# Kernel tuning notes

Hardware: AMD Instinct MI355X
Metric: run time of the kernel (lower is better)

The kernel has to match this reference:

```python
import jax, jax.numpy as jnp
import numpy as np
from jax import lax

THETA = 1.0      # neuron['theta']
TAU_SR = 10.0    # neuron['tauSr'] (SRM synaptic time constant)
TAU_RHO = 1.0    # surrogate-gradient width
SCALE_RHO = 1.0  # surrogate-gradient scale
T_SIM = 100      # simulation['tSample']


def srm_kernel(T, dtype=jnp.float32):
    t = jnp.arange(T, dtype=dtype)
    return (t / TAU_SR) * jnp.exp(1.0 - t / TAU_SR)  # eps(0)=0, peak 1 at t=tau


def psp(x, eps):
    """Causal temporal filter along last axis: y[t] = sum_k eps[k] * x[t-k]."""
    shape = x.shape
    T = shape[-1]
    xf = x.reshape(-1, 1, T)
    k = eps[::-1].reshape(1, 1, T)
    y = lax.conv_general_dilated(xf, k, (1,), [(T - 1, 0)],
                                 dimension_numbers=('NCH', 'OIH', 'NCH'))
    return y.reshape(shape)


def spike(u):
    return (u >= THETA).astype(u.dtype)


def conv_t(x, w, pad):
    """Per-timestep 2D conv. x:[B,C,H,W,T], w:[O,I,kh,kw] -> [B,O,H',W',T]."""
    B, C, H, W, T = x.shape
    xt = jnp.moveaxis(x, -1, 1).reshape(B * T, C, H, W)
    y = lax.conv_general_dilated(xt, w, (1, 1), [(pad, pad), (pad, pad)],
                                 dimension_numbers=('NCHW', 'OIHW', 'NCHW'))
    O, Ho, Wo = y.shape[1], y.shape[2], y.shape[3]
    return jnp.moveaxis(y.reshape(B, T, O, Ho, Wo), 1, -1)


def pool2(x):
    """SLAYER pool: 2x2 sum with fixed weight 1.1. x:[B,C,H,W,T]."""
    B, C, H, W, T = x.shape
    xr = x.reshape(B, C, H // 2, 2, W // 2, 2, T)
    return 1.1 * xr.sum(axis=(3, 5))


def dense_t(x, w):
    """x:[B,C,H,W,T] flattened over CHW; w:[O, C*H*W] -> [B,O,T]."""
    B = x.shape[0]
    T = x.shape[-1]
    xf = x.reshape(B, -1, T)
    return jnp.einsum('bit,oi->bot', xf, w)


def setup_inputs() -> dict:
    key = jax.random.key(0)
    k = jax.random.split(key, 6)
    img = jax.random.uniform(k[0], (32, 1, 28, 28), dtype=jnp.float32)
    rand_u = jax.random.uniform(k[1], (32, 1, 28, 28, T_SIM), dtype=jnp.float32)
    w1 = jax.random.normal(k[2], (16, 1, 5, 5), dtype=jnp.float32) * 0.2
    w2 = jax.random.normal(k[3], (32, 16, 5, 5), dtype=jnp.float32) * 0.05
    wf1 = jax.random.normal(k[4], (410, 1568), dtype=jnp.float32) * 0.05
    wf2 = jax.random.normal(k[5], (10, 410), dtype=jnp.float32) * 0.05
    return {"img": img, "rand_u": rand_u, "w1": w1, "w2": w2, "wf1": wf1, "wf2": wf2}


def reference(img, rand_u, w1, w2, wf1, wf2):
    eps = srm_kernel(T_SIM, img.dtype)
    # rate encoding: Bernoulli spikes with p = pixel intensity
    x = (rand_u < img[..., None]).astype(img.dtype)          # [B,1,28,28,T]
    x = spike(psp(conv_t(x, w1, 2), eps))                    # [B,16,28,28,T]
    x = spike(psp(pool2(x), eps))                            # [B,16,14,14,T]
    x = spike(psp(conv_t(x, w2, 2), eps))                    # [B,32,14,14,T]
    x = spike(psp(pool2(x), eps))                            # [B,32,7,7,T]
    x = spike(psp(dense_t(x, wf1), eps))                     # [B,410,T]
    x = spike(psp(jnp.einsum('bit,oi->bot', x, wf2), eps))   # [B,10,T]
    return x
```

## Files before the change

kernel.cpp:

```cpp
#include <hip/hip_runtime.h>


namespace {
constexpr int B = 32, T = 100;
constexpr double A1 = 0.90483741803595957;
constexpr double CE = 0.27182818284590452;
constexpr double SC39 = 549755813888.0;
constexpr double INV39 = 1.0 / 549755813888.0;

constexpr size_t OFF_M1 = 0;
constexpr size_t OFF_M2 = OFF_M1 + (size_t)B * T * 28 * 4;
constexpr size_t OFF_S4 = OFF_M2 + (size_t)B * T * 224 * 4;
constexpr size_t OFF_D5 = OFF_S4 + (size_t)B * T * 1568;
constexpr size_t OFF_S5 = OFF_D5 + (size_t)B * T * 410 * 8;
constexpr size_t OFF_D6 = OFF_S5 + (size_t)B * T * 410;
constexpr size_t OFF_BP = OFF_D6 + (size_t)B * T * 10 * 8;
constexpr size_t OFF_AP = OFF_D5;
}

using i32x4 = __attribute__((ext_vector_type(4))) int;
using i32x16 = __attribute__((ext_vector_type(16))) int;

__global__ void k_encode_pack(const float* __restrict__ img, const float* __restrict__ ru,
                              unsigned int* __restrict__ m1) {
  int i = blockIdx.x * 256 + threadIdx.x;
  if (i >= B * 28 * T) return;
  int t = i % T;
  int y = (i / T) % 28;
  int b = i / (T * 28);
  unsigned int m = 0;
  const float* rb = ru + ((size_t)b * 784 + y * 28) * T + t;
  const float* ib = img + b * 784 + y * 28;
  for (int x = 0; x < 28; x++) {
    m |= (rb[(size_t)x * T] < ib[x]) ? (1u << x) : 0u;
  }
  m1[((size_t)b * T + t) * 28 + y] = m;
}

__global__ __launch_bounds__(256) void k_conv1(const unsigned int* __restrict__ m1,
                                               const float* __restrict__ w1,
                                               unsigned int* __restrict__ m2) {
  __shared__ double lut[160];
  __shared__ unsigned int mrow[2][32];
  __shared__ unsigned char spk[784];
  __shared__ unsigned char spkP[2][196];
  int o = blockIdx.x % 16, b = blockIdx.x / 16;
  int tid = threadIdx.x;
  if (tid < 160) {
    int dy = tid / 32, f = tid % 32;
    double v = 0.0;
    const float* wb = w1 + o * 25 + dy * 5;
#pragma unroll
    for (int dx = 0; dx < 5; dx++)
      if ((f >> dx) & 1) v += (double)wb[dx];
    lut[tid] = v;
  }
  if (tid < 32) {
    mrow[0][tid] = 0;
    mrow[1][tid] = 0;
  }
  int y = tid / 7, xg = tid % 7;
  int py = tid / 14, px = tid % 14;
  bool act = tid < 196;
  double g1[4] = {0, 0, 0, 0}, g2[4] = {0, 0, 0, 0};
  double p1 = 0.0, p2 = 0.0;
  const unsigned int* m1b = m1 + (size_t)b * T * 28;
  if (tid < 28) mrow[0][tid + 2] = m1b[tid] << 2;
  __syncthreads();
  for (int t = 0; t < T; t++) {
    int cur = t & 1, nxt = cur ^ 1;
    bool dold = (tid < 28) && (t + 1 < T);
    unsigned int ldv = 0;
    if (dold) ldv = m1b[(t + 1) * 28 + tid] << 2;
    if (act) {
      double s0 = 0, s1 = 0, s2 = 0, s3 = 0;
      int xb = xg * 4;
      const unsigned int* mc = mrow[cur];
#pragma unroll
      for (int dy = 0; dy < 5; dy++) {
        unsigned int m = mc[y + dy];
        const double* ld = lut + dy * 32;
        s0 += ld[(m >> (xb + 0)) & 31];
        s1 += ld[(m >> (xb + 1)) & 31];
        s2 += ld[(m >> (xb + 2)) & 31];
        s3 += ld[(m >> (xb + 3)) & 31];
      }
      g1[0] = s0 + A1 * g1[0]; g2[0] = g1[0] + A1 * g2[0];
      g1[1] = s1 + A1 * g1[1]; g2[1] = g1[1] + A1 * g2[1];
      g1[2] = s2 + A1 * g1[2]; g2[2] = g1[2] + A1 * g2[2];
      g1[3] = s3 + A1 * g1[3]; g2[3] = g1[3] + A1 * g2[3];
      unsigned char* sp = spk + y * 28 + xb;
      sp[0] = (CE * (g2[0] - g1[0]) >= 1.0) ? 1 : 0;
      sp[1] = (CE * (g2[1] - g1[1]) >= 1.0) ? 1 : 0;
      sp[2] = (CE * (g2[2] - g1[2]) >= 1.0) ? 1 : 0;
      sp[3] = (CE * (g2[3] - g1[3]) >= 1.0) ? 1 : 0;
    }
    if (dold) mrow[nxt][tid + 2] = ldv;
    __syncthreads();
    if (act) {
      const unsigned char* r0 = spk + (2 * py) * 28 + 2 * px;
      int sum = (int)r0[0] + (int)r0[1] + (int)r0[28] + (int)r0[29];
      double s = 1.1 * (double)sum;
      p1 = s + A1 * p1;
      p2 = p1 + A1 * p2;
      spkP[cur][tid] = (CE * (p2 - p1) >= 1.0) ? 1 : 0;
    }
    if (tid < 14 && t > 0) {
      unsigned int m = 0;
      const unsigned char* rp = spkP[nxt] + tid * 14;
#pragma unroll
      for (int xx = 0; xx < 14; xx++) m |= ((unsigned int)rp[xx]) << xx;
      m2[((size_t)(b * T + (t - 1)) * 16 + o) * 14 + tid] = m;
    }
    __syncthreads();
  }
  if (tid < 14) {
    unsigned int m = 0;
    const unsigned char* rp = spkP[(T - 1) & 1] + tid * 14;
#pragma unroll
    for (int xx = 0; xx < 14; xx++) m |= ((unsigned int)rp[xx]) << xx;
    m2[((size_t)(b * T + (T - 1)) * 16 + o) * 14 + tid] = m;
  }
}

__global__ void k_limbs(const float* __restrict__ w2, signed char* __restrict__ AP) {
  int i = blockIdx.x * 256 + threadIdx.x;
  if (i >= 32 * 80 * 8) return;
  int dx = i & 7;
  int g = (i >> 3) % 80;
  int o = i / 640;
  int c = g >> 2, r = g & 3, eh = r >> 1, kh = r & 1;
  int lane = kh * 32 + o, e = eh * 8 + dx;
  int ci = g / 5, dy = g % 5;
  float wv = (dx < 5) ? w2[((o * 16 + ci) * 5 + dy) * 5 + dx] : 0.0f;
  long long m = llrint((double)wv * SC39);
#pragma unroll
  for (int j = 0; j < 5; j++) {
    int d = (int)((m + 128) & 255) - 128;
    AP[(size_t)((j * 20 + c) * 64 + lane) * 16 + e] = (signed char)d;
    m = (m - d) >> 8;
  }
}

__global__ __launch_bounds__(256, 1) void k_conv2u(const unsigned int* __restrict__ m2,
                                                   const signed char* __restrict__ AP,
                                                   unsigned char* __restrict__ s4) {
  __shared__ unsigned int maskW[2][2][176];
  __shared__ double part[2][2][2][32][30];
  int yp = blockIdx.x % 7, b = blockIdx.x / 7;
  int y0 = yp * 2;
  int tid = threadIdx.x;
  int w = tid >> 6, l = tid & 63;
  int tp = w >> 1, kg = w & 1;
  int col = l & 31, kh = l >> 5;
  int x = col % 14;
  unsigned int wmask = (col < 28) ? 31u : 0u;
  int half = (col >= 14) ? 1 : 0;
  const unsigned int* m2b = m2 + (size_t)b * T * 224;

  const i32x4* APv = (const i32x4*)AP;
  i32x4 Af[5][10];
#pragma unroll
  for (int j = 0; j < 5; j++)
#pragma unroll
    for (int cl = 0; cl < 10; cl++)
      Af[j][cl] = APv[(size_t)((j * 20) + kg * 10 + cl) * 64 + l];

  int stPos[3] = {-1, -1, -1}, stIdx[3] = {-1, -1, -1};
  if (w < 2) {
#pragma unroll
    for (int pass = 0; pass < 3; pass++) {
      if (pass == 2 && l >= 32) continue;
      int e = pass * 64 + l;
      int H = e / 80, g = e % 80;
      int ci = g / 5, dy = g % 5;
      int iy = y0 - 2 + H + dy;
      stPos[pass] = H * 80 + (g & 1) * 40 + 2 * (g >> 2) + ((g >> 1) & 1);
      if (iy >= 0 && iy < 14) stIdx[pass] = ci * 14 + iy;
    }
  }

  int po = tid / 7, pp = tid % 7;
  bool chainAct = tid < 224;
  double sg1[4] = {0, 0, 0, 0}, sg2[4] = {0, 0, 0, 0};
  double q1 = 0.0, q2 = 0.0;

  if (w < 2) {
#pragma unroll
    for (int pass = 0; pass < 3; pass++) {
      if (stPos[pass] < 0) continue;
      unsigned int v = 0;
      if (stIdx[pass] >= 0) v = m2b[(size_t)w * 224 + stIdx[pass]] << 2;
      maskW[0][w][stPos[pass]] = v;
    }
  }
  __syncthreads();

  for (int grp = 0; grp < 50; grp++) {
    int p = grp & 1, np = p ^ 1;

    unsigned int ld0 = 0, ld1 = 0, ld2 = 0;
    bool doStage = (w < 2) && (grp + 1 < 50);
    if (doStage) {
      size_t tb = (size_t)((grp + 1) * 2 + w) * 224;
      if (stIdx[0] >= 0) ld0 = m2b[tb + stIdx[0]] << 2;
      if (stIdx[1] >= 0) ld1 = m2b[tb + stIdx[1]] << 2;
      if (stIdx[2] >= 0) ld2 = m2b[tb + stIdx[2]] << 2;
    }

    {
      const uint4* mwv = (const uint4*)&maskW[p][tp][0];
      int base4 = half * 20 + kh * 10 + 5 * kg;
      uint4 mk0 = mwv[base4 + 0], mk1 = mwv[base4 + 1], mk2 = mwv[base4 + 2];
      uint4 mk3 = mwv[base4 + 3], mk4 = mwv[base4 + 4];
      i32x16 ac0, ac1, ac2, ac3, ac4;
#pragma unroll
      for (int r = 0; r < 16; r++) { ac0[r] = 0; ac1[r] = 0; ac2[r] = 0; ac3[r] = 0; ac4[r] = 0; }
#pragma unroll
      for (int cl = 0; cl < 10; cl++) {
        uint4 mkv = (cl < 2) ? mk0 : (cl < 4) ? mk1 : (cl < 6) ? mk2 : (cl < 8) ? mk3 : mk4;
        unsigned int ra = (cl & 1) ? mkv.z : mkv.x;
        unsigned int rb = (cl & 1) ? mkv.w : mkv.y;
        unsigned int a5 = (ra >> x) & wmask;
        unsigned int b5 = (rb >> x) & wmask;
        i32x4 bb;
        bb[0] = (int)(((a5 & 15u) * 0x204081u) & 0x01010101u);
        bb[1] = (int)((a5 >> 4) & 1u);
        bb[2] = (int)(((b5 & 15u) * 0x204081u) & 0x01010101u);
        bb[3] = (int)((b5 >> 4) & 1u);
        ac0 = __builtin_amdgcn_mfma_i32_32x32x32_i8(Af[0][cl], bb, ac0, 0, 0, 0);
        ac1 = __builtin_amdgcn_mfma_i32_32x32x32_i8(Af[1][cl], bb, ac1, 0, 0, 0);
        ac2 = __builtin_amdgcn_mfma_i32_32x32x32_i8(Af[2][cl], bb, ac2, 0, 0, 0);
        ac3 = __builtin_amdgcn_mfma_i32_32x32x32_i8(Af[3][cl], bb, ac3, 0, 0, 0);
        ac4 = __builtin_amdgcn_mfma_i32_32x32x32_i8(Af[4][cl], bb, ac4, 0, 0, 0);
      }
      if (col < 28) {
#pragma unroll
        for (int r = 0; r < 16; r++) {
          int R = (r & 3) + 8 * (r >> 2) + 4 * kh;
          int c01 = ac1[r] * 256 + ac0[r];
          int c23 = ac3[r] * 256 + ac2[r];
          double S = ((double)ac4[r] * 65536.0 + (double)c23) * 65536.0 + (double)c01;
          part[p][tp][kg][R][col] = S;
        }
      }
    }

    if (doStage) {
      if (stPos[0] >= 0) maskW[np][w][stPos[0]] = ld0;
      if (stPos[1] >= 0) maskW[np][w][stPos[1]] = ld1;
      if (stPos[2] >= 0) maskW[np][w][stPos[2]] = ld2;
    }
    __syncthreads();

    if (chainAct) {
#pragma unroll
      for (int g = 0; g < 2; g++) {
        const double* a0 = &part[p][g][0][po][2 * pp];
        const double* b0 = &part[p][g][1][po][2 * pp];
        const double* a1 = &part[p][g][0][po][14 + 2 * pp];
        const double* b1 = &part[p][g][1][po][14 + 2 * pp];
        double c0 = (a0[0] + b0[0]) * INV39;
        double c1 = (a0[1] + b0[1]) * INV39;
        double c2 = (a1[0] + b1[0]) * INV39;
        double c3 = (a1[1] + b1[1]) * INV39;
        sg1[0] = c0 + A1 * sg1[0]; sg2[0] = sg1[0] + A1 * sg2[0];
        sg1[1] = c1 + A1 * sg1[1]; sg2[1] = sg1[1] + A1 * sg2[1];
        sg1[2] = c2 + A1 * sg1[2]; sg2[2] = sg1[2] + A1 * sg2[2];
        sg1[3] = c3 + A1 * sg1[3]; sg2[3] = sg1[3] + A1 * sg2[3];
        int sum = ((CE * (sg2[0] - sg1[0]) >= 1.0) ? 1 : 0)
                + ((CE * (sg2[1] - sg1[1]) >= 1.0) ? 1 : 0)
                + ((CE * (sg2[2] - sg1[2]) >= 1.0) ? 1 : 0)
                + ((CE * (sg2[3] - sg1[3]) >= 1.0) ? 1 : 0);
        double s = 1.1 * (double)sum;
        q1 = s + A1 * q1;
        q2 = q1 + A1 * q2;
        s4[(size_t)(b * T + grp * 2 + g) * 1568 + po * 49 + yp * 7 + pp] =
            (CE * (q2 - q1) >= 1.0) ? 1 : 0;
      }
    }
  }
}

__global__ void k_limbs2(const float* __restrict__ wf1, signed char* __restrict__ BP) {
  int i = blockIdx.x * 256 + threadIdx.x;
  if (i >= 13 * 5 * 49 * 64) return;
  int lane = i & 63;
  int fi = i >> 6;
  int c = fi % 49;
  int j = (fi / 49) % 5;
  int ot = fi / 245;
  int o = ot * 32 + (lane & 31);
  int kb = 32 * c + (lane >> 5) * 16;
  int wd[4] = {0, 0, 0, 0};
#pragma unroll
  for (int e = 0; e < 16; e++) {
    float wv = (o < 410) ? wf1[(size_t)o * 1568 + kb + e] : 0.0f;
    long long m = llrint((double)wv * SC39);
    int d = 0;
    for (int jj = 0; jj <= j; jj++) {
      d = (int)((m + 128) & 255) - 128;
      m = (m - d) >> 8;
    }
    wd[e >> 2] |= (d & 255) << ((e & 3) * 8);
  }
  i32x4 v;
  v[0] = wd[0]; v[1] = wd[1]; v[2] = wd[2]; v[3] = wd[3];
  *(i32x4*)(BP + (size_t)i * 16) = v;
}

__global__ __launch_bounds__(256) void k_dense1m(const unsigned char* __restrict__ s4,
                                                 const signed char* __restrict__ BP,
                                                 double* __restrict__ d5) {
  int ot = blockIdx.y;
  int w = threadIdx.x >> 6, l = threadIdx.x & 63;
  int col = l & 31, kh = l >> 5;
  int btTile = blockIdx.x * 4 + w;
  const unsigned char* arow = s4 + (size_t)(btTile * 32 + col) * 1568 + kh * 16;
  const i32x4* bpv = (const i32x4*)BP + (size_t)ot * 245 * 64 + l;
  i32x16 acc0, acc1, acc2, acc3, acc4;
#pragma unroll
  for (int r = 0; r < 16; r++) {
    acc0[r] = 0; acc1[r] = 0; acc2[r] = 0; acc3[r] = 0; acc4[r] = 0;
  }
  for (int c = 0; c < 49; c++) {
    i32x4 a = *(const i32x4*)(arow + 32 * c);
    i32x4 b0 = bpv[(0 * 49 + c) * 64];
    i32x4 b1 = bpv[(1 * 49 + c) * 64];
    i32x4 b2 = bpv[(2 * 49 + c) * 64];
    i32x4 b3 = bpv[(3 * 49 + c) * 64];
    i32x4 b4 = bpv[(4 * 49 + c) * 64];
    acc0 = __builtin_amdgcn_mfma_i32_32x32x32_i8(a, b0, acc0, 0, 0, 0);
    acc1 = __builtin_amdgcn_mfma_i32_32x32x32_i8(a, b1, acc1, 0, 0, 0);
    acc2 = __builtin_amdgcn_mfma_i32_32x32x32_i8(a, b2, acc2, 0, 0, 0);
    acc3 = __builtin_amdgcn_mfma_i32_32x32x32_i8(a, b3, acc3, 0, 0, 0);
    acc4 = __builtin_amdgcn_mfma_i32_32x32x32_i8(a, b4, acc4, 0, 0, 0);
  }
  int o = ot * 32 + col;
  if (o < 410) {
#pragma unroll
    for (int r = 0; r < 16; r++) {
      int R = (r & 3) + 8 * (r >> 2) + 4 * kh;
      double v = ((((double)acc4[r] * 256.0 + (double)acc3[r]) * 256.0 +
                   (double)acc2[r]) * 256.0 + (double)acc1[r]) * 256.0 + (double)acc0[r];
      d5[(size_t)(btTile * 32 + R) * 410 + o] = v * INV39;
    }
  }
}

__global__ void k_psp5(const double* __restrict__ d5, unsigned char* __restrict__ s5) {
  int tid = blockIdx.x * 256 + threadIdx.x;
  if (tid >= B * 410) return;
  int o = tid % 410, b = tid / 410;
  double g1 = 0.0, g2 = 0.0;
  for (int t = 0; t < T; t++) {
    double s = d5[(size_t)(b * T + t) * 410 + o];
    g1 = s + A1 * g1;
    g2 = g1 + A1 * g2;
    s5[(size_t)(b * T + t) * 410 + o] = (CE * (g2 - g1) >= 1.0) ? 1 : 0;
  }
}

__global__ void k_dense2(const unsigned char* __restrict__ s5, const float* __restrict__ wf2,
                         double* __restrict__ d6) {
  int tid = blockIdx.x * 256 + threadIdx.x;
  if (tid >= B * T * 10) return;
  int o = tid % 10, bt = tid / 10;
  const unsigned char* sr = s5 + (size_t)bt * 410;
  const float* wr = wf2 + o * 410;
  double s = 0.0;
  for (int i = 0; i < 410; i++) s += (double)wr[i] * (double)sr[i];
  d6[tid] = s;
}

__global__ void k_psp6(const double* __restrict__ d6, float* __restrict__ out) {
  int tid = blockIdx.x * 256 + threadIdx.x;
  if (tid >= B * 10) return;
  int o = tid % 10, b = tid / 10;
  double g1 = 0.0, g2 = 0.0;
  for (int t = 0; t < T; t++) {
    double s = d6[(size_t)(b * T + t) * 10 + o];
    g1 = s + A1 * g1;
    g2 = g1 + A1 * g2;
    out[(size_t)b * 1000 + o * 100 + t] = (CE * (g2 - g1) >= 1.0) ? 1.0f : 0.0f;
  }
}

extern "C" void kernel_launch(void* const* d_in, const int* in_sizes, int n_in,
                              void* d_out, int out_size, void* d_ws, size_t ws_size,
                              hipStream_t stream) {
  const float* img = (const float*)d_in[0];
  const float* ru = (const float*)d_in[1];
  const float* w1 = (const float*)d_in[2];
  const float* w2 = (const float*)d_in[3];
  const float* wf1 = (const float*)d_in[4];
  const float* wf2 = (const float*)d_in[5];

  unsigned char* ws = (unsigned char*)d_ws;
  unsigned int* m1 = (unsigned int*)(ws + OFF_M1);
  unsigned int* m2 = (unsigned int*)(ws + OFF_M2);
  unsigned char* s4 = ws + OFF_S4;
  double* d5 = (double*)(ws + OFF_D5);
  unsigned char* s5 = ws + OFF_S5;
  double* d6 = (double*)(ws + OFF_D6);
  signed char* AP = (signed char*)(ws + OFF_AP);
  signed char* BP = (signed char*)(ws + OFF_BP);
  float* out = (float*)d_out;

  k_encode_pack<<<(B * 28 * T + 255) / 256, 256, 0, stream>>>(img, ru, m1);
  k_limbs<<<(32 * 80 * 8 + 255) / 256, 256, 0, stream>>>(w2, AP);
  k_limbs2<<<(13 * 5 * 49 * 64 + 255) / 256, 256, 0, stream>>>(wf1, BP);
  k_conv1<<<B * 16, 256, 0, stream>>>(m1, w1, m2);
  k_conv2u<<<B * 7, 256, 0, stream>>>(m2, AP, s4);
  k_dense1m<<<dim3(25, 13), 256, 0, stream>>>(s4, BP, d5);
  k_psp5<<<(B * 410 + 255) / 256, 256, 0, stream>>>(d5, s5);
  k_dense2<<<(B * T * 10 + 255) / 256, 256, 0, stream>>>(s5, wf2, d6);
  k_psp6<<<2, 256, 0, stream>>>(d6, out);
}
```

Before: 404.8 us.

## Split conv2 K-reduction across four wave groups in 512-thread blocks

The conv2 kernel now runs 512 threads per block: eight waves split the channel reduction into four K-quarters per time step instead of two halves. Each wave holds half as many A-fragment registers and issues half as many MFMAs per step. The PSP chain moves to the upper 256 threads and sums four partials. The partial buffer loses its double buffering and an extra barrier is added per iteration, which serializes MFMA work and the chain update, but the aim is more waves in flight and shorter per-wave MFMA sequences.

```diff
diff --git a/kernel.cpp b/kernel.cpp
--- a/kernel.cpp
+++ b/kernel.cpp
@@ -142,16 +142,16 @@
   }
 }
 
-__global__ __launch_bounds__(256, 1) void k_conv2u(const unsigned int* __restrict__ m2,
+__global__ __launch_bounds__(512, 2) void k_conv2w(const unsigned int* __restrict__ m2,
                                                    const signed char* __restrict__ AP,
                                                    unsigned char* __restrict__ s4) {
-  __shared__ unsigned int maskW[2][2][176];
-  __shared__ double part[2][2][2][32][30];
+  __shared__ unsigned int maskW[2][2][192];
+  __shared__ double part[2][4][32][30];
   int yp = blockIdx.x % 7, b = blockIdx.x / 7;
   int y0 = yp * 2;
   int tid = threadIdx.x;
   int w = tid >> 6, l = tid & 63;
-  int tp = w >> 1, kg = w & 1;
+  int tp = w & 1, kq = w >> 1;
   int col = l & 31, kh = l >> 5;
   int x = col % 14;
   unsigned int wmask = (col < 28) ? 31u : 0u;
@@ -159,12 +159,12 @@
   const unsigned int* m2b = m2 + (size_t)b * T * 224;
 
   const i32x4* APv = (const i32x4*)AP;
-  i32x4 Af[5][10];
+  i32x4 Af[5][5];
 #pragma unroll
   for (int j = 0; j < 5; j++)
 #pragma unroll
-    for (int cl = 0; cl < 10; cl++)
-      Af[j][cl] = APv[(size_t)((j * 20) + kg * 10 + cl) * 64 + l];
+    for (int q = 0; q < 5; q++)
+      Af[j][q] = APv[(size_t)(j * 20 + 5 * kq + q) * 64 + l];
 
   int stPos[3] = {-1, -1, -1}, stIdx[3] = {-1, -1, -1};
   if (w < 2) {
@@ -173,17 +173,21 @@
       if (pass == 2 && l >= 32) continue;
       int e = pass * 64 + l;
       int H = e / 80, g = e % 80;
+      int c = g >> 2, eh2 = (g >> 1) & 1, kh2 = g & 1;
+      int kq2 = c / 5, q2 = c % 5;
       int ci = g / 5, dy = g % 5;
       int iy = y0 - 2 + H + dy;
-      stPos[pass] = H * 80 + (g & 1) * 40 + 2 * (g >> 2) + ((g >> 1) & 1);
+      stPos[pass] = H * 96 + kh2 * 48 + kq2 * 12 + q2 * 2 + eh2;
       if (iy >= 0 && iy < 14) stIdx[pass] = ci * 14 + iy;
     }
   }
 
-  int po = tid / 7, pp = tid % 7;
-  bool chainAct = tid < 224;
+  int ct = tid - 256;
+  bool chainAct = (ct >= 0) && (ct < 224);
+  int po = (ct >= 0) ? ct / 7 : 0;
+  int pp = (ct >= 0) ? ct % 7 : 0;
   double sg1[4] = {0, 0, 0, 0}, sg2[4] = {0, 0, 0, 0};
-  double q1 = 0.0, q2 = 0.0;
+  double pq1 = 0.0, pq2 = 0.0;
 
   if (w < 2) {
 #pragma unroll
@@ -210,17 +214,17 @@
 
     {
       const uint4* mwv = (const uint4*)&maskW[p][tp][0];
-      int base4 = half * 20 + kh * 10 + 5 * kg;
+      int base4 = half * 24 + kh * 12 + kq * 3;
       uint4 mk0 = mwv[base4 + 0], mk1 = mwv[base4 + 1], mk2 = mwv[base4 + 2];
-      uint4 mk3 = mwv[base4 + 3], mk4 = mwv[base4 + 4];
       i32x16 ac0, ac1, ac2, ac3, ac4;
 #pragma unroll
       for (int r = 0; r < 16; r++) { ac0[r] = 0; ac1[r] = 0; ac2[r] = 0; ac3[r] = 0; ac4[r] = 0; }
 #pragma unroll
-      for (int cl = 0; cl < 10; cl++) {
-        uint4 mkv = (cl < 2) ? mk0 : (cl < 4) ? mk1 : (cl < 6) ? mk2 : (cl < 8) ? mk3 : mk4;
-        unsigned int ra = (cl & 1) ? mkv.z : mkv.x;
-        unsigned int rb = (cl & 1) ? mkv.w : mkv.y;
+      for (int q = 0; q < 5; q++) {
+        unsigned int ra = (q == 0) ? mk0.x : (q == 1) ? mk0.z : (q == 2) ? mk1.x
+                         : (q == 3) ? mk1.z : mk2.x;
+        unsigned int rb = (q == 0) ? mk0.y : (q == 1) ? mk0.w : (q == 2) ? mk1.y
+                         : (q == 3) ? mk1.w : mk2.y;
         unsigned int a5 = (ra >> x) & wmask;
         unsigned int b5 = (rb >> x) & wmask;
         i32x4 bb;
@@ -228,11 +232,11 @@
         bb[1] = (int)((a5 >> 4) & 1u);
         bb[2] = (int)(((b5 & 15u) * 0x204081u) & 0x01010101u);
         bb[3] = (int)((b5 >> 4) & 1u);
-        ac0 = __builtin_amdgcn_mfma_i32_32x32x32_i8(Af[0][cl], bb, ac0, 0, 0, 0);
-        ac1 = __builtin_amdgcn_mfma_i32_32x32x32_i8(Af[1][cl], bb, ac1, 0, 0, 0);
-        ac2 = __builtin_amdgcn_mfma_i32_32x32x32_i8(Af[2][cl], bb, ac2, 0, 0, 0);
-        ac3 = __builtin_amdgcn_mfma_i32_32x32x32_i8(Af[3][cl], bb, ac3, 0, 0, 0);
-        ac4 = __builtin_amdgcn_mfma_i32_32x32x32_i8(Af[4][cl], bb, ac4, 0, 0, 0);
+        ac0 = __builtin_amdgcn_mfma_i32_32x32x32_i8(Af[0][q], bb, ac0, 0, 0, 0);
+        ac1 = __builtin_amdgcn_mfma_i32_32x32x32_i8(Af[1][q], bb, ac1, 0, 0, 0);
+        ac2 = __builtin_amdgcn_mfma_i32_32x32x32_i8(Af[2][q], bb, ac2, 0, 0, 0);
+        ac3 = __builtin_amdgcn_mfma_i32_32x32x32_i8(Af[3][q], bb, ac3, 0, 0, 0);
+        ac4 = __builtin_amdgcn_mfma_i32_32x32x32_i8(Af[4][q], bb, ac4, 0, 0, 0);
       }
       if (col < 28) {
 #pragma unroll
@@ -241,7 +245,7 @@
           int c01 = ac1[r] * 256 + ac0[r];
           int c23 = ac3[r] * 256 + ac2[r];
           double S = ((double)ac4[r] * 65536.0 + (double)c23) * 65536.0 + (double)c01;
-          part[p][tp][kg][R][col] = S;
+          part[tp][kq][R][col] = S;
         }
       }
     }
@@ -256,14 +260,18 @@
     if (chainAct) {
 #pragma unroll
       for (int g = 0; g < 2; g++) {
-        const double* a0 = &part[p][g][0][po][2 * pp];
-        const double* b0 = &part[p][g][1][po][2 * pp];
-        const double* a1 = &part[p][g][0][po][14 + 2 * pp];
-        const double* b1 = &part[p][g][1][po][14 + 2 * pp];
-        double c0 = (a0[0] + b0[0]) * INV39;
-        double c1 = (a0[1] + b0[1]) * INV39;
-        double c2 = (a1[0] + b1[0]) * INV39;
-        double c3 = (a1[1] + b1[1]) * INV39;
+        const double* q0a = &part[g][0][po][2 * pp];
+        const double* q1a = &part[g][1][po][2 * pp];
+        const double* q2a = &part[g][2][po][2 * pp];
+        const double* q3a = &part[g][3][po][2 * pp];
+        const double* q0b = &part[g][0][po][14 + 2 * pp];
+        const double* q1b = &part[g][1][po][14 + 2 * pp];
+        const double* q2b = &part[g][2][po][14 + 2 * pp];
+        const double* q3b = &part[g][3][po][14 + 2 * pp];
+        double c0 = ((q0a[0] + q1a[0]) + (q2a[0] + q3a[0])) * INV39;
+        double c1 = ((q0a[1] + q1a[1]) + (q2a[1] + q3a[1])) * INV39;
+        double c2 = ((q0b[0] + q1b[0]) + (q2b[0] + q3b[0])) * INV39;
+        double c3 = ((q0b[1] + q1b[1]) + (q2b[1] + q3b[1])) * INV39;
         sg1[0] = c0 + A1 * sg1[0]; sg2[0] = sg1[0] + A1 * sg2[0];
         sg1[1] = c1 + A1 * sg1[1]; sg2[1] = sg1[1] + A1 * sg2[1];
         sg1[2] = c2 + A1 * sg1[2]; sg2[2] = sg1[2] + A1 * sg2[2];
@@ -273,12 +281,13 @@
                 + ((CE * (sg2[2] - sg1[2]) >= 1.0) ? 1 : 0)
                 + ((CE * (sg2[3] - sg1[3]) >= 1.0) ? 1 : 0);
         double s = 1.1 * (double)sum;
-        q1 = s + A1 * q1;
-        q2 = q1 + A1 * q2;
+        pq1 = s + A1 * pq1;
+        pq2 = pq1 + A1 * pq2;
         s4[(size_t)(b * T + grp * 2 + g) * 1568 + po * 49 + yp * 7 + pp] =
-            (CE * (q2 - q1) >= 1.0) ? 1 : 0;
+            (CE * (pq2 - pq1) >= 1.0) ? 1 : 0;
       }
     }
+    __syncthreads();
   }
 }
 
@@ -411,7 +420,7 @@
   k_limbs<<<(32 * 80 * 8 + 255) / 256, 256, 0, stream>>>(w2, AP);
   k_limbs2<<<(13 * 5 * 49 * 64 + 255) / 256, 256, 0, stream>>>(wf1, BP);
   k_conv1<<<B * 16, 256, 0, stream>>>(m1, w1, m2);
-  k_conv2u<<<B * 7, 256, 0, stream>>>(m2, AP, s4);
+  k_conv2w<<<B * 7, 512, 0, stream>>>(m2, AP, s4);
   k_dense1m<<<dim3(25, 13), 256, 0, stream>>>(s4, BP, d5);
   k_psp5<<<(B * 410 + 255) / 256, 256, 0, stream>>>(d5, s5);
   k_dense2<<<(B * T * 10 + 255) / 256, 256, 0, stream>>>(s5, wf2, d6);
```

Result: faster. 376.0 us (-7.1%).
